# Kernel tuning notes

Measured on AMD Instinct MI355X. Metric: run time of the kernel, lower is better.

## Reference

```python
import jax, jax.numpy as jnp
import numpy as np

NUM_CLASSES = 4
NUM_PROTOTYPE = 8
D = 512
N = 200704  # 16 * 112 * 112 flattened tokens
GAMMA = 0.999        # EMA momentum (self.gamma)
EPS_SINK = 0.05      # sinkhorn epsilon
SINK_ITERS = 3       # sinkhorn iterations


def l2_normalize(x, axis=-1, eps=1e-12):
    n = jnp.linalg.norm(x, axis=axis, keepdims=True)
    return x / jnp.maximum(n, eps)


def layer_norm(x, g, b, eps=1e-5):
    mu = jnp.mean(x, axis=-1, keepdims=True)
    var = jnp.var(x, axis=-1, keepdims=True)
    return (x - mu) / jnp.sqrt(var + eps) * g + b


def masked_sinkhorn(scores, sel):
    # scores: [N, M] similarity to this class's prototypes; sel: [N] bool row mask
    # Faithful masked re-expression of distributed_sinkhorn (which gathers rows
    # where gt_seg == k); zeroed rows contribute nothing to any normalization.
    M = scores.shape[1]
    self32 = sel.astype(scores.dtype)[:, None]
    L = jnp.exp(scores / EPS_SINK) * self32           # [N, M]
    B = jnp.maximum(sel.sum(), 1).astype(scores.dtype)  # number of selected rows
    L = L / jnp.maximum(L.sum(), 1e-30)

    def body(L, _):
        col = L.sum(axis=0, keepdims=True)            # per-prototype mass
        L = L / jnp.maximum(col, 1e-30) / M
        row = L.sum(axis=1, keepdims=True)            # per-token mass
        L = (L / jnp.maximum(row, 1e-30) / B) * self32
        return L, None

    L, _ = jax.lax.scan(body, L, None, length=SINK_ITERS)
    L = L * B
    idx = jnp.argmax(L, axis=1)
    # hard one-hot assignment (deterministic stand-in for hard gumbel_softmax)
    q = jax.nn.one_hot(idx, M, dtype=scores.dtype) * self32
    return q


def prototype_learning(_c, pred, gt_seg, masks, protos, momentum):
    # _c [N, D], pred/gt_seg [N], masks [N, M, K], protos [K, M, D]
    correct = gt_seg == pred
    new_rows = []
    for k in range(NUM_CLASSES):  # small fixed class loop, as in the original
        sel = gt_seg == k
        q = masked_sinkhorn(masks[:, :, k], sel)      # [N, M]
        m_k = (correct & sel).astype(_c.dtype)        # [N]
        m_q = q * m_k[:, None]                        # masked assignments
        c_q = _c * m_k[:, None]                       # masked features
        f = m_q.T @ c_q                               # [M, D] aggregation
        n = m_q.sum(axis=0)                           # [M] per-prototype counts
        f = l2_normalize(f)
        upd = momentum * protos[k] + (1.0 - momentum) * f
        valid = (n != 0) & (sel.sum() > 0) & (n.sum() > 0)
        new_rows.append(jnp.where(valid[:, None], upd, protos[k]))
    return l2_normalize(jnp.stack(new_rows, axis=0))


def reference(feats, ln_gamma, ln_beta, mask_gamma, mask_beta, prototypes, gt_seg):
    _c = l2_normalize(layer_norm(feats, ln_gamma, ln_beta))       # [N, D]
    protos = l2_normalize(prototypes)                             # [K, M, D]
    masks = jnp.einsum('nd,kmd->nmk', _c, protos)                 # [N, M, K]
    out_seg = layer_norm(jnp.max(masks, axis=1), mask_gamma, mask_beta)  # [N, K]
    pred = jnp.argmax(out_seg, axis=1)
    new_protos = prototype_learning(_c, pred, gt_seg.astype(jnp.int32), masks, protos, GAMMA)
    return out_seg, new_protos


def setup_inputs() -> dict:
    key = jax.random.key(0)
    k1, k2, k3 = jax.random.split(key, 3)
    return {
        'feats': jax.random.normal(k1, (N, D), dtype=jnp.float32),
        'ln_gamma': jnp.ones((D,), jnp.float32),
        'ln_beta': jnp.zeros((D,), jnp.float32),
        'mask_gamma': jnp.ones((NUM_CLASSES,), jnp.float32),
        'mask_beta': jnp.zeros((NUM_CLASSES,), jnp.float32),
        'prototypes': 0.02 * jax.random.normal(k2, (NUM_CLASSES, NUM_PROTOTYPE, D), dtype=jnp.float32),
        'gt_seg': jax.random.randint(k3, (N,), 0, NUM_CLASSES, dtype=jnp.int32),
    }
```

## Files before the change

kernel.cpp:

```cpp
#include <hip/hip_runtime.h>
#include <hip/hip_bf16.h>
#include <math.h>

#define NROWS 200704
#define DIM 512
#define NKM 32

#define OFF_RED0   0
#define OFF_RED1   32
#define OFF_RED2   64
#define OFF_CNT    96
#define OFF_NP     100
#define OFF_CUR    192
#define OFF_BASE   2240
#define OFF_FACC   2304
#define ZERO_FLOATS 18688
#define OFF_SUMGP  18688
#define OFF_BP     18720
#define OFF_SCAL   18752
#define OFF_G2GB   18816
#define OFF_PROTON 19840
#define OFF_WHI    36224
#define OFF_WLO    44544
#define OFF_RSTATS 52864
#define OFF_E      855680
#define OFF_FLAGS  2461312
#define OFF_SORT   2662016

typedef __attribute__((ext_vector_type(8)))  short short8;
typedef __attribute__((ext_vector_type(16))) float f32x16;

union ABFrag { unsigned int u[4]; short8 s; };

__device__ __forceinline__ unsigned int pk2(float a, float b) {
    __hip_bfloat162 h2 = __float22bfloat162_rn(make_float2(a, b));
    union { __hip_bfloat162 h; unsigned int u; } cv;
    cv.h = h2;
    return cv.u;
}

__device__ __forceinline__ float block_reduce_sum(float v, float* sm) {
    int t = threadIdx.x;
    sm[t] = v; __syncthreads();
    #pragma unroll
    for (int o = 128; o > 0; o >>= 1) {
        if (t < o) sm[t] += sm[t + o];
        __syncthreads();
    }
    float r = sm[0]; __syncthreads();
    return r;
}

__global__ __launch_bounds__(256) void k_prep(const float* __restrict__ protos,
                                              const float* __restrict__ g,
                                              const float* __restrict__ b,
                                              float* __restrict__ ws) {
    __shared__ float sm[256];
    int t = threadIdx.x, j = blockIdx.x;
    if (j < NKM) {
        const float* p = protos + j * DIM;
        float v = p[t] * p[t] + p[t + 256] * p[t + 256];
        float ss = block_reduce_sum(v, sm);
        float den = fmaxf(sqrtf(ss), 1e-12f);
        float sgp = 0.f, sbp = 0.f;
        unsigned short* whi = (unsigned short*)ws + 2 * OFF_WHI + j * 520;
        unsigned short* wlo = (unsigned short*)ws + 2 * OFF_WLO + j * 520;
        for (int d = t; d < DIM; d += 256) {
            float pn = p[d] / den;
            ws[OFF_PROTON + j * DIM + d] = pn;
            float w = g[d] * pn;
            unsigned int hb = pk2(w, 0.f) & 0xffffu;
            float hf = __uint_as_float(hb << 16);
            unsigned int lb = pk2(w - hf, 0.f) & 0xffffu;
            whi[d] = (unsigned short)hb;
            wlo[d] = (unsigned short)lb;
            sgp += w; sbp += b[d] * pn;
        }
        float s1 = block_reduce_sum(sgp, sm);
        float s2 = block_reduce_sum(sbp, sm);
        if (t == 0) { ws[OFF_SUMGP + j] = s1; ws[OFF_BP + j] = s2; }
    } else {
        float a = 0.f, c = 0.f, e = 0.f;
        for (int d = t; d < DIM; d += 256) {
            float gv = g[d], bv = b[d];
            ws[OFF_G2GB + 2 * d]     = gv * gv;
            ws[OFF_G2GB + 2 * d + 1] = gv * bv;
            a += gv * gv; c += gv * bv; e += bv * bv;
        }
        float s1 = block_reduce_sum(a, sm);
        float s2 = block_reduce_sum(c, sm);
        float s3 = block_reduce_sum(e, sm);
        if (t == 0) { ws[OFF_SCAL] = s1; ws[OFF_SCAL + 1] = s2; ws[OFF_SCAL + 2] = s3; }
    }
}

#define ST1(XV, G2V, GBV) { float _x = (XV); float _x2 = _x * _x; \
    sx += _x; sxx += _x2; \
    sxg2  = fmaf(_x,  (G2V), sxg2); \
    sx2g2 = fmaf(_x2, (G2V), sx2g2); \
    sxgb  = fmaf(_x,  (GBV), sxgb); }

#define PAIRSPLIT(A0, B0, HO, LO) { \
    unsigned int _h = pk2((A0), (B0)); HO = _h; \
    float _ha = __uint_as_float(_h << 16); \
    float _hb = __uint_as_float(_h & 0xffff0000u); \
    LO = pk2((A0) - _ha, (B0) - _hb); }

__global__ __launch_bounds__(1024, 4) void k_main(const float* __restrict__ feats,
                                                  const float* __restrict__ mg,
                                                  const float* __restrict__ mb,
                                                  const int* __restrict__ gt_seg,
                                                  float* __restrict__ ws,
                                                  float* __restrict__ out) {
    __shared__ __align__(16) unsigned short ls_whi[32 * 520];
    __shared__ __align__(16) unsigned short ls_wlo[32 * 520];
    __shared__ __align__(16) float ls_g2gb[1024];
    __shared__ float s_lred[NKM];
    __shared__ int s_lcnt[4];
    int t = threadIdx.x;
    {
        const float4* sh = (const float4*)(ws + OFF_WHI);
        float4* dh = (float4*)ls_whi;
        for (int i = t; i < 2080; i += 1024) dh[i] = sh[i];
        const float4* sl = (const float4*)(ws + OFF_WLO);
        float4* dl = (float4*)ls_wlo;
        for (int i = t; i < 2080; i += 1024) dl[i] = sl[i];
        if (t < 256) ((float4*)ls_g2gb)[t] = ((const float4*)(ws + OFF_G2GB))[t];
        if (t < NKM) s_lred[t] = 0.f;
        if (t < 4) s_lcnt[t] = 0;
    }
    __syncthreads();

    int wv = t >> 6, l = t & 63;
    int h = l >> 5, c32 = l & 31;
    int row0 = blockIdx.x * 512 + wv * 32;
    const float* xrow = feats + (size_t)(row0 + c32) * DIM + h * 8;
    const unsigned short* bhp = ls_whi + c32 * 520 + h * 8;
    const unsigned short* blp = ls_wlo + c32 * 520 + h * 8;
    const float4* g4 = ((const float4*)ls_g2gb) + h * 4;

    f32x16 acc;
    #pragma unroll
    for (int i = 0; i < 16; ++i) acc[i] = 0.f;
    float sx = 0.f, sxx = 0.f, sxg2 = 0.f, sx2g2 = 0.f, sxgb = 0.f;

    #pragma unroll 2
    for (int kc = 0; kc < 32; ++kc) {
        float4 xa = *(const float4*)(xrow + kc * 16);
        float4 xb = *(const float4*)(xrow + kc * 16 + 4);
        float4 ga  = g4[kc * 8 + 0];
        float4 gb_ = g4[kc * 8 + 1];
        float4 gc  = g4[kc * 8 + 2];
        float4 gd  = g4[kc * 8 + 3];
        ST1(xa.x, ga.x,  ga.y)  ST1(xa.y, ga.z,  ga.w)
        ST1(xa.z, gb_.x, gb_.y) ST1(xa.w, gb_.z, gb_.w)
        ST1(xb.x, gc.x,  gc.y)  ST1(xb.y, gc.z,  gc.w)
        ST1(xb.z, gd.x,  gd.y)  ST1(xb.w, gd.z,  gd.w)
        ABFrag ah, al;
        PAIRSPLIT(xa.x, xa.y, ah.u[0], al.u[0])
        PAIRSPLIT(xa.z, xa.w, ah.u[1], al.u[1])
        PAIRSPLIT(xb.x, xb.y, ah.u[2], al.u[2])
        PAIRSPLIT(xb.z, xb.w, ah.u[3], al.u[3])
        short8 bh = *(const short8*)(bhp + kc * 16);
        short8 bl = *(const short8*)(blp + kc * 16);
        acc = __builtin_amdgcn_mfma_f32_32x32x16_bf16(ah.s, bh, acc, 0, 0, 0);
        acc = __builtin_amdgcn_mfma_f32_32x32x16_bf16(ah.s, bl, acc, 0, 0, 0);
        acc = __builtin_amdgcn_mfma_f32_32x32x16_bf16(al.s, bh, acc, 0, 0, 0);
    }

    sx    += __shfl_xor(sx, 32, 64);
    sxx   += __shfl_xor(sxx, 32, 64);
    sxg2  += __shfl_xor(sxg2, 32, 64);
    sx2g2 += __shfl_xor(sx2g2, 32, 64);
    sxgb  += __shfl_xor(sxgb, 32, 64);

    float scal0 = ws[OFF_SCAL], scal1 = ws[OFF_SCAL + 1], scal2 = ws[OFF_SCAL + 2];
    float mu  = sx * (1.0f / DIM);
    float var = sxx * (1.0f / DIM) - mu * mu;
    float istd = 1.0f / sqrtf(var + 1e-5f);
    float l2v = istd * istd * (sx2g2 - 2.0f * mu * sxg2 + mu * mu * scal0)
              + 2.0f * istd * (sxgb - mu * scal1) + scal2;
    float L = sqrtf(fmaxf(l2v, 0.0f));
    float invL = 1.0f / fmaxf(L, 1e-12f);
    float aa = istd * invL;
    if (l < 32)
        *(float4*)(ws + OFF_RSTATS + (size_t)(row0 + l) * 4) = make_float4(mu, istd, invL, 0.f);

    float wsum = ws[OFF_SUMGP + c32], wbp = ws[OFF_BP + c32];
    float mg0 = mg[0], mg1 = mg[1], mg2 = mg[2], mg3 = mg[3];
    float mb0 = mb[0], mb1 = mb[1], mb2 = mb[2], mb3 = mb[3];
    int q = c32 >> 3;
    int li8 = c32 & 7;

    #pragma unroll
    for (int r = 0; r < 16; ++r) {
        int rowt = (r & 3) + 8 * (r >> 2) + 4 * h;
        int grow = row0 + rowt;
        float mu_r = __shfl(mu, rowt, 64);
        float aa_r = __shfl(aa, rowt, 64);
        float il_r = __shfl(invL, rowt, 64);
        float s = aa_r * (acc[r] - mu_r * wsum) + il_r * wbp;
        float m = s;
        m = fmaxf(m, __shfl_xor(m, 1, 64));
        m = fmaxf(m, __shfl_xor(m, 2, 64));
        m = fmaxf(m, __shfl_xor(m, 4, 64));
        float vA = m;
        float vB = __shfl_xor(vA, 8, 64);
        float vC = __shfl_xor(vA, 16, 64);
        float vD = __shfl_xor(vB, 16, 64);
        float o0 = (q == 0) ? vA : (q == 1) ? vB : (q == 2) ? vC : vD;
        float o1 = (q == 1) ? vA : (q == 0) ? vB : (q == 3) ? vC : vD;
        float o2 = (q == 2) ? vA : (q == 3) ? vB : (q == 0) ? vC : vD;
        float o3 = (q == 3) ? vA : (q == 2) ? vB : (q == 1) ? vC : vD;
        float mu4 = 0.25f * (o0 + o1 + o2 + o3);
        float e0 = o0 - mu4, e1 = o1 - mu4, e2 = o2 - mu4, e3 = o3 - mu4;
        float v4 = 0.25f * (e0 * e0 + e1 * e1 + e2 * e2 + e3 * e3);
        float is4 = 1.0f / sqrtf(v4 + 1e-5f);
        float f0 = e0 * is4 * mg0 + mb0;
        float f1 = e1 * is4 * mg1 + mb1;
        float f2 = e2 * is4 * mg2 + mb2;
        float f3 = e3 * is4 * mg3 + mb3;
        int pred = 0; float bo = f0;
        if (f1 > bo) { bo = f1; pred = 1; }
        if (f2 > bo) { bo = f2; pred = 2; }
        if (f3 > bo) { bo = f3; pred = 3; }
        int gtv = gt_seg[grow] & 3;
        if (c32 == 0) {
            *(float4*)(out + (size_t)grow * 4) = make_float4(f0, f1, f2, f3);
            ((int*)ws)[OFF_FLAGS + grow] = gtv | ((pred == gtv) ? 4 : 0);
        }
        if (q == gtv) {
            float ev = expf(s * 20.0f);
            ws[OFF_E + (size_t)grow * 8 + li8] = ev;
            atomicAdd(&s_lred[(q << 3) + li8], ev);
            if (li8 == 0) atomicAdd(&s_lcnt[q], 1);
        }
    }
    __syncthreads();
    if (t < NKM) atomicAdd(&ws[OFF_RED0 + t], s_lred[t]);
    if (t < 4) atomicAdd(&((int*)ws)[OFF_CNT + t], s_lcnt[t]);
}

__global__ __launch_bounds__(256) void k_red1(const int* __restrict__ gt_seg,
                                              float* __restrict__ ws) {
    __shared__ float S0p[4], Bk[4], a1[NKM], lred[NKM];
    int t = threadIdx.x;
    if (t < 4) {
        float s = 0.f;
        #pragma unroll
        for (int m = 0; m < 8; ++m) s += ws[OFF_RED0 + t * 8 + m];
        S0p[t] = fmaxf(s, 1e-30f);
        Bk[t] = fmaxf((float)((const int*)ws)[OFF_CNT + t], 1.0f);
    }
    if (t < NKM) lred[t] = 0.f;
    __syncthreads();
    if (t < NKM) {
        float col = ws[OFF_RED0 + t] / S0p[t >> 3];
        a1[t] = 1.0f / (fmaxf(col, 1e-30f) * 8.0f);
    }
    __syncthreads();
    int row = blockIdx.x * 256 + t;
    int gt = gt_seg[row] & 3;
    float4 ea = *(const float4*)(ws + OFF_E + (size_t)row * 8);
    float4 eb = *(const float4*)(ws + OFF_E + (size_t)row * 8 + 4);
    float ev[8] = {ea.x, ea.y, ea.z, ea.w, eb.x, eb.y, eb.z, eb.w};
    float dotv = 0.f;
    #pragma unroll
    for (int m = 0; m < 8; ++m) dotv += ev[m] * a1[gt * 8 + m];
    float row1 = dotv / S0p[gt];
    float r1 = 1.0f / (fmaxf(row1, 1e-30f) * Bk[gt]);
    #pragma unroll
    for (int m = 0; m < 8; ++m) atomicAdd(&lred[gt * 8 + m], ev[m] * r1);
    __syncthreads();
    if (t < NKM) atomicAdd(&ws[OFF_RED1 + t], lred[t]);
}

__global__ __launch_bounds__(256) void k_red2(const int* __restrict__ gt_seg,
                                              float* __restrict__ ws) {
    __shared__ float S0p[4], Bk[4], a1[NKM], a2[NKM], lred[NKM];
    int t = threadIdx.x;
    if (t < 4) {
        float s = 0.f;
        #pragma unroll
        for (int m = 0; m < 8; ++m) s += ws[OFF_RED0 + t * 8 + m];
        S0p[t] = fmaxf(s, 1e-30f);
        Bk[t] = fmaxf((float)((const int*)ws)[OFF_CNT + t], 1.0f);
    }
    if (t < NKM) lred[t] = 0.f;
    __syncthreads();
    if (t < NKM) {
        float col = ws[OFF_RED0 + t] / S0p[t >> 3];
        a1[t] = 1.0f / (fmaxf(col, 1e-30f) * 8.0f);
    }
    __syncthreads();
    if (t < NKM) {
        float col2 = a1[t] * ws[OFF_RED1 + t] / S0p[t >> 3];
        a2[t] = 1.0f / (fmaxf(col2, 1e-30f) * 8.0f);
    }
    __syncthreads();
    int row = blockIdx.x * 256 + t;
    int gt = gt_seg[row] & 3;
    float4 ea = *(const float4*)(ws + OFF_E + (size_t)row * 8);
    float4 eb = *(const float4*)(ws + OFF_E + (size_t)row * 8 + 4);
    float ev[8] = {ea.x, ea.y, ea.z, ea.w, eb.x, eb.y, eb.z, eb.w};
    float dotv = 0.f;
    #pragma unroll
    for (int m = 0; m < 8; ++m) dotv += ev[m] * a1[gt * 8 + m];
    float row1 = dotv / S0p[gt];
    float r1 = 1.0f / (fmaxf(row1, 1e-30f) * Bk[gt]);
    float dot2 = 0.f;
    #pragma unroll
    for (int m = 0; m < 8; ++m) dot2 += ev[m] * a1[gt * 8 + m] * a2[gt * 8 + m];
    float row2 = dot2 / S0p[gt] * r1;
    float r2 = 1.0f / (fmaxf(row2, 1e-30f) * Bk[gt]);
    #pragma unroll
    for (int m = 0; m < 8; ++m) atomicAdd(&lred[gt * 8 + m], ev[m] * r1 * r2);
    __syncthreads();
    if (t < NKM) atomicAdd(&ws[OFF_RED2 + t], lred[t]);
}

__global__ __launch_bounds__(256) void k_assign(float* __restrict__ ws) {
    __shared__ float S0p[4], Bk[4], a1[NKM], a2[NKM], F[NKM];
    __shared__ int ln[NKM];
    int t = threadIdx.x;
    if (t < 4) {
        float s = 0.f;
        #pragma unroll
        for (int m = 0; m < 8; ++m) s += ws[OFF_RED0 + t * 8 + m];
        S0p[t] = fmaxf(s, 1e-30f);
        Bk[t] = fmaxf((float)((const int*)ws)[OFF_CNT + t], 1.0f);
    }
    if (t < NKM) ln[t] = 0;
    __syncthreads();
    if (t < NKM) {
        float col = ws[OFF_RED0 + t] / S0p[t >> 3];
        a1[t] = 1.0f / (fmaxf(col, 1e-30f) * 8.0f);
    }
    __syncthreads();
    if (t < NKM) {
        float col2 = a1[t] * ws[OFF_RED1 + t] / S0p[t >> 3];
        a2[t] = 1.0f / (fmaxf(col2, 1e-30f) * 8.0f);
    }
    __syncthreads();
    if (t < NKM) {
        float col3 = a1[t] * a2[t] * ws[OFF_RED2 + t] / S0p[t >> 3];
        float a3 = 1.0f / (fmaxf(col3, 1e-30f) * 8.0f);
        F[t] = a1[t] * a2[t] * a3;
    }
    __syncthreads();
    int row = blockIdx.x * 256 + t;
    int flag = ((const int*)ws)[OFF_FLAGS + row];
    int slotv = -1;
    if (flag & 4) {
        int gt = flag & 3;
        float4 ea = *(const float4*)(ws + OFF_E + (size_t)row * 8);
        float4 eb = *(const float4*)(ws + OFF_E + (size_t)row * 8 + 4);
        float ev[8] = {ea.x, ea.y, ea.z, ea.w, eb.x, eb.y, eb.z, eb.w};
        int js = 0; float bv = ev[0] * F[gt * 8];
        #pragma unroll
        for (int m = 1; m < 8; ++m) {
            float v = ev[m] * F[gt * 8 + m];
            if (v > bv) { bv = v; js = m; }
        }
        slotv = gt * 8 + js;
        atomicAdd(&ln[slotv], 1);
    }
    ((int*)ws)[OFF_FLAGS + row] = slotv;
    __syncthreads();
    if (t < NKM && ln[t]) atomicAdd(&((int*)ws)[OFF_NP + t], ln[t]);
}

__global__ __launch_bounds__(256) void k_scatter(float* __restrict__ ws) {
    __shared__ int s_base[NKM];
    int t = threadIdx.x;
    if (t == 0) {
        int acc = 0;
        #pragma unroll
        for (int s = 0; s < NKM; ++s) { s_base[s] = acc; acc += ((const int*)ws)[OFF_NP + s]; }
    }
    __syncthreads();
    int row = blockIdx.x * 256 + t;
    int s = ((const int*)ws)[OFF_FLAGS + row];
    if (s >= 0) {
        int pos = atomicAdd(&((int*)ws)[OFF_CUR + s * 64], 1);
        ((int*)ws)[OFF_SORT + s_base[s] + pos] = row;
    }
}

__global__ __launch_bounds__(256) void k_agg(const float* __restrict__ feats,
                                             const float* __restrict__ g,
                                             const float* __restrict__ b,
                                             float* __restrict__ ws) {
    __shared__ int s_bn[2];
    int t = threadIdx.x;
    int slot = blockIdx.x >> 4, ch = blockIdx.x & 15;
    if (t == 0) {
        int acc = 0;
        for (int s = 0; s < slot; ++s) acc += ((const int*)ws)[OFF_NP + s];
        s_bn[0] = acc;
        s_bn[1] = ((const int*)ws)[OFF_NP + slot];
    }
    __syncthreads();
    int base = s_bn[0], n = s_bn[1];
    int r0 = base + (ch * n) / 16;
    int r1 = base + ((ch + 1) * n) / 16;
    if (r0 >= r1) return;
    const int* sortl = (const int*)ws + OFF_SORT;
    float2 gv = *(const float2*)(g + 2 * t);
    float2 bv = *(const float2*)(b + 2 * t);
    float acc0 = 0.f, acc1 = 0.f;
    #pragma unroll 4
    for (int i = r0; i < r1; ++i) {
        int row = sortl[i];
        float4 rs = *(const float4*)(ws + OFF_RSTATS + (size_t)row * 4);
        float2 x = *(const float2*)(feats + (size_t)row * DIM + 2 * t);
        acc0 += ((x.x - rs.x) * rs.y * gv.x + bv.x) * rs.z;
        acc1 += ((x.y - rs.x) * rs.y * gv.y + bv.y) * rs.z;
    }
    atomicAdd(&ws[OFF_FACC + slot * DIM + 2 * t],     acc0);
    atomicAdd(&ws[OFF_FACC + slot * DIM + 2 * t + 1], acc1);
}

__global__ __launch_bounds__(256) void k_final(float* __restrict__ ws,
                                               float* __restrict__ out) {
    __shared__ float sm[256];
    int t = threadIdx.x, j = blockIdx.x, k = j >> 3;
    int nj = ((const int*)ws)[OFF_NP + j];
    int ck = ((const int*)ws)[OFF_CNT + k];
    int nsum = 0;
    #pragma unroll
    for (int m = 0; m < 8; ++m) nsum += ((const int*)ws)[OFF_NP + k * 8 + m];
    int d0 = t, d1 = t + 256;
    float f0 = ws[OFF_FACC + j * DIM + d0];
    float f1 = ws[OFF_FACC + j * DIM + d1];
    float nf = block_reduce_sum(f0 * f0 + f1 * f1, sm);
    float fin = 1.0f / fmaxf(sqrtf(nf), 1e-12f);
    float pn0 = ws[OFF_PROTON + j * DIM + d0];
    float pn1 = ws[OFF_PROTON + j * DIM + d1];
    bool valid = (nj != 0) && (ck > 0) && (nsum > 0);
    float r0 = valid ? (0.999f * pn0 + 0.001f * (f0 * fin)) : pn0;
    float r1 = valid ? (0.999f * pn1 + 0.001f * (f1 * fin)) : pn1;
    float n2 = block_reduce_sum(r0 * r0 + r1 * r1, sm);
    float i2 = 1.0f / fmaxf(sqrtf(n2), 1e-12f);
    out[(size_t)NROWS * 4 + j * DIM + d0] = r0 * i2;
    out[(size_t)NROWS * 4 + j * DIM + d1] = r1 * i2;
}

extern "C" void kernel_launch(void* const* d_in, const int* in_sizes, int n_in,
                              void* d_out, int out_size, void* d_ws, size_t ws_size,
                              hipStream_t stream) {
    const float* feats = (const float*)d_in[0];
    const float* ln_g  = (const float*)d_in[1];
    const float* ln_b  = (const float*)d_in[2];
    const float* mg    = (const float*)d_in[3];
    const float* mb    = (const float*)d_in[4];
    const float* prot  = (const float*)d_in[5];
    const int*   gt    = (const int*)d_in[6];
    float* out = (float*)d_out;
    float* ws  = (float*)d_ws;

    hipMemsetAsync(d_ws, 0, ZERO_FLOATS * 4, stream);
    k_prep<<<33, 256, 0, stream>>>(prot, ln_g, ln_b, ws);
    k_main<<<NROWS / 512, 1024, 0, stream>>>(feats, mg, mb, gt, ws, out);
    k_red1<<<NROWS / 256, 256, 0, stream>>>(gt, ws);
    k_red2<<<NROWS / 256, 256, 0, stream>>>(gt, ws);
    k_assign<<<NROWS / 256, 256, 0, stream>>>(ws);
    k_scatter<<<NROWS / 256, 256, 0, stream>>>(ws);
    k_agg<<<NKM * 16, 256, 0, stream>>>(feats, ln_g, ln_b, ws);
    k_final<<<NKM, 256, 0, stream>>>(ws, out);
}
```

Measured before the change: 681.7 us.

## Fuse sinkhorn, assign, scatter, aggregate and final into one cooperative kernel

Replaces the six post-main kernels with a single cooperative-launch kernel that uses grid-wide syncs between phases. Each thread loads its row's exp scores, gt and flag once and keeps them in registers for all phases. This removes repeated global re-reads, the flag write-back and several launch gaps. The aggregation split per slot goes from 16 to 24 chunks. In exchange the kernel adds four grid barriers and needs all 784 blocks to be co-resident, which the occupancy hint on the launch bounds is meant to guarantee.

```diff
diff --git a/kernel.cpp b/kernel.cpp
--- a/kernel.cpp
+++ b/kernel.cpp
@@ -1,6 +1,9 @@
 #include <hip/hip_runtime.h>
+#include <hip/hip_cooperative_groups.h>
 #include <hip/hip_bf16.h>
 #include <math.h>
+
+namespace cg = cooperative_groups;
 
 #define NROWS 200704
 #define DIM 512
@@ -241,10 +244,24 @@
     if (t < 4) atomicAdd(&((int*)ws)[OFF_CNT + t], s_lcnt[t]);
 }
 
-__global__ __launch_bounds__(256) void k_red1(const int* __restrict__ gt_seg,
-                                              float* __restrict__ ws) {
-    __shared__ float S0p[4], Bk[4], a1[NKM], lred[NKM];
+__global__ __launch_bounds__(256, 4) void k_sink(const float* __restrict__ feats,
+                                                 const float* __restrict__ g,
+                                                 const float* __restrict__ b,
+                                                 const int* __restrict__ gt_seg,
+                                                 float* __restrict__ ws,
+                                                 float* __restrict__ out) {
+    cg::grid_group grid = cg::this_grid();
+    __shared__ float S0p[4], Bk[4], a1[NKM], a2[NKM], F[NKM], lred[NKM];
+    __shared__ int ln[NKM], s_np[NKM], s_base[NKM];
+    __shared__ float sm[256];
     int t = threadIdx.x;
+    int row = blockIdx.x * 256 + t;
+    int gt = gt_seg[row] & 3;
+    float4 ea = *(const float4*)(ws + OFF_E + (size_t)row * 8);
+    float4 eb = *(const float4*)(ws + OFF_E + (size_t)row * 8 + 4);
+    float ev[8] = {ea.x, ea.y, ea.z, ea.w, eb.x, eb.y, eb.z, eb.w};
+    int flag = ((const int*)ws)[OFF_FLAGS + row];
+
     if (t < 4) {
         float s = 0.f;
         #pragma unroll
@@ -259,11 +276,6 @@
         a1[t] = 1.0f / (fmaxf(col, 1e-30f) * 8.0f);
     }
     __syncthreads();
-    int row = blockIdx.x * 256 + t;
-    int gt = gt_seg[row] & 3;
-    float4 ea = *(const float4*)(ws + OFF_E + (size_t)row * 8);
-    float4 eb = *(const float4*)(ws + OFF_E + (size_t)row * 8 + 4);
-    float ev[8] = {ea.x, ea.y, ea.z, ea.w, eb.x, eb.y, eb.z, eb.w};
     float dotv = 0.f;
     #pragma unroll
     for (int m = 0; m < 8; ++m) dotv += ev[m] * a1[gt * 8 + m];
@@ -273,41 +285,15 @@
     for (int m = 0; m < 8; ++m) atomicAdd(&lred[gt * 8 + m], ev[m] * r1);
     __syncthreads();
     if (t < NKM) atomicAdd(&ws[OFF_RED1 + t], lred[t]);
-}
-
-__global__ __launch_bounds__(256) void k_red2(const int* __restrict__ gt_seg,
-                                              float* __restrict__ ws) {
-    __shared__ float S0p[4], Bk[4], a1[NKM], a2[NKM], lred[NKM];
-    int t = threadIdx.x;
-    if (t < 4) {
-        float s = 0.f;
-        #pragma unroll
-        for (int m = 0; m < 8; ++m) s += ws[OFF_RED0 + t * 8 + m];
-        S0p[t] = fmaxf(s, 1e-30f);
-        Bk[t] = fmaxf((float)((const int*)ws)[OFF_CNT + t], 1.0f);
-    }
+    grid.sync();
+
     if (t < NKM) lred[t] = 0.f;
-    __syncthreads();
-    if (t < NKM) {
-        float col = ws[OFF_RED0 + t] / S0p[t >> 3];
-        a1[t] = 1.0f / (fmaxf(col, 1e-30f) * 8.0f);
-    }
     __syncthreads();
     if (t < NKM) {
         float col2 = a1[t] * ws[OFF_RED1 + t] / S0p[t >> 3];
         a2[t] = 1.0f / (fmaxf(col2, 1e-30f) * 8.0f);
     }
     __syncthreads();
-    int row = blockIdx.x * 256 + t;
-    int gt = gt_seg[row] & 3;
-    float4 ea = *(const float4*)(ws + OFF_E + (size_t)row * 8);
-    float4 eb = *(const float4*)(ws + OFF_E + (size_t)row * 8 + 4);
-    float ev[8] = {ea.x, ea.y, ea.z, ea.w, eb.x, eb.y, eb.z, eb.w};
-    float dotv = 0.f;
-    #pragma unroll
-    for (int m = 0; m < 8; ++m) dotv += ev[m] * a1[gt * 8 + m];
-    float row1 = dotv / S0p[gt];
-    float r1 = 1.0f / (fmaxf(row1, 1e-30f) * Bk[gt]);
     float dot2 = 0.f;
     #pragma unroll
     for (int m = 0; m < 8; ++m) dot2 += ev[m] * a1[gt * 8 + m] * a2[gt * 8 + m];
@@ -317,30 +303,9 @@
     for (int m = 0; m < 8; ++m) atomicAdd(&lred[gt * 8 + m], ev[m] * r1 * r2);
     __syncthreads();
     if (t < NKM) atomicAdd(&ws[OFF_RED2 + t], lred[t]);
-}
-
-__global__ __launch_bounds__(256) void k_assign(float* __restrict__ ws) {
-    __shared__ float S0p[4], Bk[4], a1[NKM], a2[NKM], F[NKM];
-    __shared__ int ln[NKM];
-    int t = threadIdx.x;
-    if (t < 4) {
-        float s = 0.f;
-        #pragma unroll
-        for (int m = 0; m < 8; ++m) s += ws[OFF_RED0 + t * 8 + m];
-        S0p[t] = fmaxf(s, 1e-30f);
-        Bk[t] = fmaxf((float)((const int*)ws)[OFF_CNT + t], 1.0f);
-    }
+    grid.sync();
+
     if (t < NKM) ln[t] = 0;
-    __syncthreads();
-    if (t < NKM) {
-        float col = ws[OFF_RED0 + t] / S0p[t >> 3];
-        a1[t] = 1.0f / (fmaxf(col, 1e-30f) * 8.0f);
-    }
-    __syncthreads();
-    if (t < NKM) {
-        float col2 = a1[t] * ws[OFF_RED1 + t] / S0p[t >> 3];
-        a2[t] = 1.0f / (fmaxf(col2, 1e-30f) * 8.0f);
-    }
     __syncthreads();
     if (t < NKM) {
         float col3 = a1[t] * a2[t] * ws[OFF_RED2 + t] / S0p[t >> 3];
@@ -348,14 +313,8 @@
         F[t] = a1[t] * a2[t] * a3;
     }
     __syncthreads();
-    int row = blockIdx.x * 256 + t;
-    int flag = ((const int*)ws)[OFF_FLAGS + row];
     int slotv = -1;
     if (flag & 4) {
-        int gt = flag & 3;
-        float4 ea = *(const float4*)(ws + OFF_E + (size_t)row * 8);
-        float4 eb = *(const float4*)(ws + OFF_E + (size_t)row * 8 + 4);
-        float ev[8] = {ea.x, ea.y, ea.z, ea.w, eb.x, eb.y, eb.z, eb.w};
         int js = 0; float bv = ev[0] * F[gt * 8];
         #pragma unroll
         for (int m = 1; m < 8; ++m) {
@@ -365,85 +324,70 @@
         slotv = gt * 8 + js;
         atomicAdd(&ln[slotv], 1);
     }
-    ((int*)ws)[OFF_FLAGS + row] = slotv;
     __syncthreads();
     if (t < NKM && ln[t]) atomicAdd(&((int*)ws)[OFF_NP + t], ln[t]);
-}
-
-__global__ __launch_bounds__(256) void k_scatter(float* __restrict__ ws) {
-    __shared__ int s_base[NKM];
-    int t = threadIdx.x;
+    grid.sync();
+
+    if (t < NKM) s_np[t] = ((const int*)ws)[OFF_NP + t];
+    __syncthreads();
     if (t == 0) {
         int acc = 0;
         #pragma unroll
-        for (int s = 0; s < NKM; ++s) { s_base[s] = acc; acc += ((const int*)ws)[OFF_NP + s]; }
-    }
-    __syncthreads();
-    int row = blockIdx.x * 256 + t;
-    int s = ((const int*)ws)[OFF_FLAGS + row];
-    if (s >= 0) {
-        int pos = atomicAdd(&((int*)ws)[OFF_CUR + s * 64], 1);
-        ((int*)ws)[OFF_SORT + s_base[s] + pos] = row;
-    }
-}
-
-__global__ __launch_bounds__(256) void k_agg(const float* __restrict__ feats,
-                                             const float* __restrict__ g,
-                                             const float* __restrict__ b,
-                                             float* __restrict__ ws) {
-    __shared__ int s_bn[2];
-    int t = threadIdx.x;
-    int slot = blockIdx.x >> 4, ch = blockIdx.x & 15;
-    if (t == 0) {
-        int acc = 0;
-        for (int s = 0; s < slot; ++s) acc += ((const int*)ws)[OFF_NP + s];
-        s_bn[0] = acc;
-        s_bn[1] = ((const int*)ws)[OFF_NP + slot];
-    }
-    __syncthreads();
-    int base = s_bn[0], n = s_bn[1];
-    int r0 = base + (ch * n) / 16;
-    int r1 = base + ((ch + 1) * n) / 16;
-    if (r0 >= r1) return;
-    const int* sortl = (const int*)ws + OFF_SORT;
-    float2 gv = *(const float2*)(g + 2 * t);
-    float2 bv = *(const float2*)(b + 2 * t);
-    float acc0 = 0.f, acc1 = 0.f;
-    #pragma unroll 4
-    for (int i = r0; i < r1; ++i) {
-        int row = sortl[i];
-        float4 rs = *(const float4*)(ws + OFF_RSTATS + (size_t)row * 4);
-        float2 x = *(const float2*)(feats + (size_t)row * DIM + 2 * t);
-        acc0 += ((x.x - rs.x) * rs.y * gv.x + bv.x) * rs.z;
-        acc1 += ((x.y - rs.x) * rs.y * gv.y + bv.y) * rs.z;
-    }
-    atomicAdd(&ws[OFF_FACC + slot * DIM + 2 * t],     acc0);
-    atomicAdd(&ws[OFF_FACC + slot * DIM + 2 * t + 1], acc1);
-}
-
-__global__ __launch_bounds__(256) void k_final(float* __restrict__ ws,
-                                               float* __restrict__ out) {
-    __shared__ float sm[256];
-    int t = threadIdx.x, j = blockIdx.x, k = j >> 3;
-    int nj = ((const int*)ws)[OFF_NP + j];
-    int ck = ((const int*)ws)[OFF_CNT + k];
-    int nsum = 0;
-    #pragma unroll
-    for (int m = 0; m < 8; ++m) nsum += ((const int*)ws)[OFF_NP + k * 8 + m];
-    int d0 = t, d1 = t + 256;
-    float f0 = ws[OFF_FACC + j * DIM + d0];
-    float f1 = ws[OFF_FACC + j * DIM + d1];
-    float nf = block_reduce_sum(f0 * f0 + f1 * f1, sm);
-    float fin = 1.0f / fmaxf(sqrtf(nf), 1e-12f);
-    float pn0 = ws[OFF_PROTON + j * DIM + d0];
-    float pn1 = ws[OFF_PROTON + j * DIM + d1];
-    bool valid = (nj != 0) && (ck > 0) && (nsum > 0);
-    float r0 = valid ? (0.999f * pn0 + 0.001f * (f0 * fin)) : pn0;
-    float r1 = valid ? (0.999f * pn1 + 0.001f * (f1 * fin)) : pn1;
-    float n2 = block_reduce_sum(r0 * r0 + r1 * r1, sm);
-    float i2 = 1.0f / fmaxf(sqrtf(n2), 1e-12f);
-    out[(size_t)NROWS * 4 + j * DIM + d0] = r0 * i2;
-    out[(size_t)NROWS * 4 + j * DIM + d1] = r1 * i2;
+        for (int s2 = 0; s2 < NKM; ++s2) { s_base[s2] = acc; acc += s_np[s2]; }
+    }
+    __syncthreads();
+    if (slotv >= 0) {
+        int pos = atomicAdd(&((int*)ws)[OFF_CUR + slotv * 64], 1);
+        ((int*)ws)[OFF_SORT + s_base[slotv] + pos] = row;
+    }
+    grid.sync();
+
+    if (blockIdx.x < NKM * 24) {
+        int slot = blockIdx.x / 24, ch = blockIdx.x % 24;
+        int n = s_np[slot], base = s_base[slot];
+        int r0 = base + (ch * n) / 24;
+        int r1e = base + ((ch + 1) * n) / 24;
+        if (r0 < r1e) {
+            const int* sortl = (const int*)ws + OFF_SORT;
+            float2 gv = *(const float2*)(g + 2 * t);
+            float2 bv = *(const float2*)(b + 2 * t);
+            float acc0 = 0.f, acc1 = 0.f;
+            #pragma unroll 4
+            for (int i = r0; i < r1e; ++i) {
+                int rr = sortl[i];
+                float4 rs = *(const float4*)(ws + OFF_RSTATS + (size_t)rr * 4);
+                float2 x = *(const float2*)(feats + (size_t)rr * DIM + 2 * t);
+                acc0 += ((x.x - rs.x) * rs.y * gv.x + bv.x) * rs.z;
+                acc1 += ((x.y - rs.x) * rs.y * gv.y + bv.y) * rs.z;
+            }
+            atomicAdd(&ws[OFF_FACC + slot * DIM + 2 * t],     acc0);
+            atomicAdd(&ws[OFF_FACC + slot * DIM + 2 * t + 1], acc1);
+        }
+    }
+    grid.sync();
+
+    if (blockIdx.x < NKM) {
+        int j = blockIdx.x, k = j >> 3;
+        int nj = s_np[j];
+        int ck = ((const int*)ws)[OFF_CNT + k];
+        int nsum = 0;
+        #pragma unroll
+        for (int m = 0; m < 8; ++m) nsum += s_np[k * 8 + m];
+        int d0 = t, d1 = t + 256;
+        float f0 = ws[OFF_FACC + j * DIM + d0];
+        float f1 = ws[OFF_FACC + j * DIM + d1];
+        float nf = block_reduce_sum(f0 * f0 + f1 * f1, sm);
+        float fin = 1.0f / fmaxf(sqrtf(nf), 1e-12f);
+        float pn0 = ws[OFF_PROTON + j * DIM + d0];
+        float pn1 = ws[OFF_PROTON + j * DIM + d1];
+        bool valid = (nj != 0) && (ck > 0) && (nsum > 0);
+        float rr0 = valid ? (0.999f * pn0 + 0.001f * (f0 * fin)) : pn0;
+        float rr1 = valid ? (0.999f * pn1 + 0.001f * (f1 * fin)) : pn1;
+        float n2 = block_reduce_sum(rr0 * rr0 + rr1 * rr1, sm);
+        float i2 = 1.0f / fmaxf(sqrtf(n2), 1e-12f);
+        out[(size_t)NROWS * 4 + j * DIM + d0] = rr0 * i2;
+        out[(size_t)NROWS * 4 + j * DIM + d1] = rr1 * i2;
+    }
 }
 
 extern "C" void kernel_launch(void* const* d_in, const int* in_sizes, int n_in,
@@ -462,10 +406,8 @@
     hipMemsetAsync(d_ws, 0, ZERO_FLOATS * 4, stream);
     k_prep<<<33, 256, 0, stream>>>(prot, ln_g, ln_b, ws);
     k_main<<<NROWS / 512, 1024, 0, stream>>>(feats, mg, mb, gt, ws, out);
-    k_red1<<<NROWS / 256, 256, 0, stream>>>(gt, ws);
-    k_red2<<<NROWS / 256, 256, 0, stream>>>(gt, ws);
-    k_assign<<<NROWS / 256, 256, 0, stream>>>(ws);
-    k_scatter<<<NROWS / 256, 256, 0, stream>>>(ws);
-    k_agg<<<NKM * 16, 256, 0, stream>>>(feats, ln_g, ln_b, ws);
-    k_final<<<NKM, 256, 0, stream>>>(ws, out);
-}
+    void* args[] = { (void*)&feats, (void*)&ln_g, (void*)&ln_b,
+                     (void*)&gt, (void*)&ws, (void*)&out };
+    hipLaunchCooperativeKernel(reinterpret_cast<void*>(k_sink),
+                               dim3(NROWS / 256), dim3(256), args, 0, stream);
+}
```

New measurement: 1.051 ms. 1.54x slower.

## Fuse scatter into assign with per-slot buckets and batch reduction rows per block

Applied to the files above, without the earlier changes.

The assign kernel now appends each selected row index straight into a per-slot bucket (fixed capacity of NROWS per slot) through an atomic counter, so the separate count-then-scatter kernel and the prefix sum over slot counts go away. The aggregation and final kernels read the per-slot counts from the counters. The two Sinkhorn reduction kernels also process four rows per thread with a quarter of the blocks, which cuts shared and global atomic traffic per row. The cost is a much larger workspace region for the buckets and more global atomics concentrated on 32 counters inside the assign kernel.

```diff
diff --git a/kernel.cpp b/kernel.cpp
--- a/kernel.cpp
+++ b/kernel.cpp
@@ -25,7 +25,7 @@
 #define OFF_RSTATS 52864
 #define OFF_E      855680
 #define OFF_FLAGS  2461312
-#define OFF_SORT   2662016
+#define OFF_BUCKET 4000000
 
 typedef __attribute__((ext_vector_type(8)))  short short8;
 typedef __attribute__((ext_vector_type(16))) float f32x16;
@@ -259,18 +259,21 @@
         a1[t] = 1.0f / (fmaxf(col, 1e-30f) * 8.0f);
     }
     __syncthreads();
-    int row = blockIdx.x * 256 + t;
-    int gt = gt_seg[row] & 3;
-    float4 ea = *(const float4*)(ws + OFF_E + (size_t)row * 8);
-    float4 eb = *(const float4*)(ws + OFF_E + (size_t)row * 8 + 4);
-    float ev[8] = {ea.x, ea.y, ea.z, ea.w, eb.x, eb.y, eb.z, eb.w};
-    float dotv = 0.f;
-    #pragma unroll
-    for (int m = 0; m < 8; ++m) dotv += ev[m] * a1[gt * 8 + m];
-    float row1 = dotv / S0p[gt];
-    float r1 = 1.0f / (fmaxf(row1, 1e-30f) * Bk[gt]);
-    #pragma unroll
-    for (int m = 0; m < 8; ++m) atomicAdd(&lred[gt * 8 + m], ev[m] * r1);
+    #pragma unroll
+    for (int i = 0; i < 4; ++i) {
+        int row = blockIdx.x * 1024 + i * 256 + t;
+        int gt = gt_seg[row] & 3;
+        float4 ea = *(const float4*)(ws + OFF_E + (size_t)row * 8);
+        float4 eb = *(const float4*)(ws + OFF_E + (size_t)row * 8 + 4);
+        float ev[8] = {ea.x, ea.y, ea.z, ea.w, eb.x, eb.y, eb.z, eb.w};
+        float dotv = 0.f;
+        #pragma unroll
+        for (int m = 0; m < 8; ++m) dotv += ev[m] * a1[gt * 8 + m];
+        float row1 = dotv / S0p[gt];
+        float r1 = 1.0f / (fmaxf(row1, 1e-30f) * Bk[gt]);
+        #pragma unroll
+        for (int m = 0; m < 8; ++m) atomicAdd(&lred[gt * 8 + m], ev[m] * r1);
+    }
     __syncthreads();
     if (t < NKM) atomicAdd(&ws[OFF_RED1 + t], lred[t]);
 }
@@ -298,39 +301,39 @@
         a2[t] = 1.0f / (fmaxf(col2, 1e-30f) * 8.0f);
     }
     __syncthreads();
-    int row = blockIdx.x * 256 + t;
-    int gt = gt_seg[row] & 3;
-    float4 ea = *(const float4*)(ws + OFF_E + (size_t)row * 8);
-    float4 eb = *(const float4*)(ws + OFF_E + (size_t)row * 8 + 4);
-    float ev[8] = {ea.x, ea.y, ea.z, ea.w, eb.x, eb.y, eb.z, eb.w};
-    float dotv = 0.f;
-    #pragma unroll
-    for (int m = 0; m < 8; ++m) dotv += ev[m] * a1[gt * 8 + m];
-    float row1 = dotv / S0p[gt];
-    float r1 = 1.0f / (fmaxf(row1, 1e-30f) * Bk[gt]);
-    float dot2 = 0.f;
-    #pragma unroll
-    for (int m = 0; m < 8; ++m) dot2 += ev[m] * a1[gt * 8 + m] * a2[gt * 8 + m];
-    float row2 = dot2 / S0p[gt] * r1;
-    float r2 = 1.0f / (fmaxf(row2, 1e-30f) * Bk[gt]);
-    #pragma unroll
-    for (int m = 0; m < 8; ++m) atomicAdd(&lred[gt * 8 + m], ev[m] * r1 * r2);
+    #pragma unroll
+    for (int i = 0; i < 4; ++i) {
+        int row = blockIdx.x * 1024 + i * 256 + t;
+        int gt = gt_seg[row] & 3;
+        float4 ea = *(const float4*)(ws + OFF_E + (size_t)row * 8);
+        float4 eb = *(const float4*)(ws + OFF_E + (size_t)row * 8 + 4);
+        float ev[8] = {ea.x, ea.y, ea.z, ea.w, eb.x, eb.y, eb.z, eb.w};
+        float dotv = 0.f;
+        #pragma unroll
+        for (int m = 0; m < 8; ++m) dotv += ev[m] * a1[gt * 8 + m];
+        float row1 = dotv / S0p[gt];
+        float r1 = 1.0f / (fmaxf(row1, 1e-30f) * Bk[gt]);
+        float dot2 = 0.f;
+        #pragma unroll
+        for (int m = 0; m < 8; ++m) dot2 += ev[m] * a1[gt * 8 + m] * a2[gt * 8 + m];
+        float row2 = dot2 / S0p[gt] * r1;
+        float r2 = 1.0f / (fmaxf(row2, 1e-30f) * Bk[gt]);
+        #pragma unroll
+        for (int m = 0; m < 8; ++m) atomicAdd(&lred[gt * 8 + m], ev[m] * r1 * r2);
+    }
     __syncthreads();
     if (t < NKM) atomicAdd(&ws[OFF_RED2 + t], lred[t]);
 }
 
 __global__ __launch_bounds__(256) void k_assign(float* __restrict__ ws) {
-    __shared__ float S0p[4], Bk[4], a1[NKM], a2[NKM], F[NKM];
-    __shared__ int ln[NKM];
+    __shared__ float S0p[4], a1[NKM], a2[NKM], F[NKM];
     int t = threadIdx.x;
     if (t < 4) {
         float s = 0.f;
         #pragma unroll
         for (int m = 0; m < 8; ++m) s += ws[OFF_RED0 + t * 8 + m];
         S0p[t] = fmaxf(s, 1e-30f);
-        Bk[t] = fmaxf((float)((const int*)ws)[OFF_CNT + t], 1.0f);
-    }
-    if (t < NKM) ln[t] = 0;
+    }
     __syncthreads();
     if (t < NKM) {
         float col = ws[OFF_RED0 + t] / S0p[t >> 3];
@@ -350,7 +353,6 @@
     __syncthreads();
     int row = blockIdx.x * 256 + t;
     int flag = ((const int*)ws)[OFF_FLAGS + row];
-    int slotv = -1;
     if (flag & 4) {
         int gt = flag & 3;
         float4 ea = *(const float4*)(ws + OFF_E + (size_t)row * 8);
@@ -362,28 +364,9 @@
             float v = ev[m] * F[gt * 8 + m];
             if (v > bv) { bv = v; js = m; }
         }
-        slotv = gt * 8 + js;
-        atomicAdd(&ln[slotv], 1);
-    }
-    ((int*)ws)[OFF_FLAGS + row] = slotv;
-    __syncthreads();
-    if (t < NKM && ln[t]) atomicAdd(&((int*)ws)[OFF_NP + t], ln[t]);
-}
-
-__global__ __launch_bounds__(256) void k_scatter(float* __restrict__ ws) {
-    __shared__ int s_base[NKM];
-    int t = threadIdx.x;
-    if (t == 0) {
-        int acc = 0;
-        #pragma unroll
-        for (int s = 0; s < NKM; ++s) { s_base[s] = acc; acc += ((const int*)ws)[OFF_NP + s]; }
-    }
-    __syncthreads();
-    int row = blockIdx.x * 256 + t;
-    int s = ((const int*)ws)[OFF_FLAGS + row];
-    if (s >= 0) {
-        int pos = atomicAdd(&((int*)ws)[OFF_CUR + s * 64], 1);
-        ((int*)ws)[OFF_SORT + s_base[s] + pos] = row;
+        int slotv = gt * 8 + js;
+        int pos = atomicAdd(&((int*)ws)[OFF_CUR + slotv * 64], 1);
+        ((int*)ws)[OFF_BUCKET + (size_t)slotv * NROWS + pos] = row;
     }
 }
 
@@ -391,27 +374,19 @@
                                              const float* __restrict__ g,
                                              const float* __restrict__ b,
                                              float* __restrict__ ws) {
-    __shared__ int s_bn[2];
     int t = threadIdx.x;
     int slot = blockIdx.x >> 4, ch = blockIdx.x & 15;
-    if (t == 0) {
-        int acc = 0;
-        for (int s = 0; s < slot; ++s) acc += ((const int*)ws)[OFF_NP + s];
-        s_bn[0] = acc;
-        s_bn[1] = ((const int*)ws)[OFF_NP + slot];
-    }
-    __syncthreads();
-    int base = s_bn[0], n = s_bn[1];
-    int r0 = base + (ch * n) / 16;
-    int r1 = base + ((ch + 1) * n) / 16;
+    int n = ((const int*)ws)[OFF_CUR + slot * 64];
+    int r0 = (ch * n) / 16;
+    int r1 = ((ch + 1) * n) / 16;
     if (r0 >= r1) return;
-    const int* sortl = (const int*)ws + OFF_SORT;
+    const int* bucket = (const int*)ws + OFF_BUCKET + (size_t)slot * NROWS;
     float2 gv = *(const float2*)(g + 2 * t);
     float2 bv = *(const float2*)(b + 2 * t);
     float acc0 = 0.f, acc1 = 0.f;
     #pragma unroll 4
     for (int i = r0; i < r1; ++i) {
-        int row = sortl[i];
+        int row = bucket[i];
         float4 rs = *(const float4*)(ws + OFF_RSTATS + (size_t)row * 4);
         float2 x = *(const float2*)(feats + (size_t)row * DIM + 2 * t);
         acc0 += ((x.x - rs.x) * rs.y * gv.x + bv.x) * rs.z;
@@ -425,11 +400,11 @@
                                                float* __restrict__ out) {
     __shared__ float sm[256];
     int t = threadIdx.x, j = blockIdx.x, k = j >> 3;
-    int nj = ((const int*)ws)[OFF_NP + j];
+    int nj = ((const int*)ws)[OFF_CUR + j * 64];
     int ck = ((const int*)ws)[OFF_CNT + k];
     int nsum = 0;
     #pragma unroll
-    for (int m = 0; m < 8; ++m) nsum += ((const int*)ws)[OFF_NP + k * 8 + m];
+    for (int m = 0; m < 8; ++m) nsum += ((const int*)ws)[OFF_CUR + (k * 8 + m) * 64];
     int d0 = t, d1 = t + 256;
     float f0 = ws[OFF_FACC + j * DIM + d0];
     float f1 = ws[OFF_FACC + j * DIM + d1];
@@ -462,10 +437,9 @@
     hipMemsetAsync(d_ws, 0, ZERO_FLOATS * 4, stream);
     k_prep<<<33, 256, 0, stream>>>(prot, ln_g, ln_b, ws);
     k_main<<<NROWS / 512, 1024, 0, stream>>>(feats, mg, mb, gt, ws, out);
-    k_red1<<<NROWS / 256, 256, 0, stream>>>(gt, ws);
-    k_red2<<<NROWS / 256, 256, 0, stream>>>(gt, ws);
+    k_red1<<<196, 256, 0, stream>>>(gt, ws);
+    k_red2<<<196, 256, 0, stream>>>(gt, ws);
     k_assign<<<NROWS / 256, 256, 0, stream>>>(ws);
-    k_scatter<<<NROWS / 256, 256, 0, stream>>>(ws);
     k_agg<<<NKM * 16, 256, 0, stream>>>(feats, ln_g, ln_b, ws);
     k_final<<<NKM, 256, 0, stream>>>(ws, out);
 }
```

Result: no change. 670.6 us (-1.6%).
